# Optimization experiments

Hardware: AMD Instinct MI355X
Metric: run time of the kernel (lower is better)

## Reference

```python
import jax, jax.numpy as jnp
import numpy as np

B, N, S, D1, D2 = 8, 16384, 1024, 256, 256
C_IN, C_MID, C_OUT = D1 + D2, 256, 256
BN_EPS = 1e-5
DIST_EPS = 1e-8


def setup_inputs() -> dict:
    key = jax.random.key(0)
    ks = jax.random.split(key, 12)
    return {
        "xyz1": jax.random.normal(ks[0], (B, 3, N), jnp.float32),
        "xyz2": jax.random.normal(ks[1], (B, 3, S), jnp.float32),
        "points1": jax.random.normal(ks[2], (B, D1, N), jnp.float32),
        "points2": jax.random.normal(ks[3], (B, D2, S), jnp.float32),
        "w0": jax.random.normal(ks[4], (C_MID, C_IN), jnp.float32) * (1.0 / np.sqrt(C_IN)),
        "b0": jnp.zeros((C_MID,), jnp.float32),
        "g0": jnp.ones((C_MID,), jnp.float32),
        "be0": jnp.zeros((C_MID,), jnp.float32),
        "w1": jax.random.normal(ks[5], (C_OUT, C_MID), jnp.float32) * (1.0 / np.sqrt(C_MID)),
        "b1": jnp.zeros((C_OUT,), jnp.float32),
        "g1": jnp.ones((C_OUT,), jnp.float32),
        "be1": jnp.zeros((C_OUT,), jnp.float32),
    }


def _propagate(xyz1, xyz2, points1, points2):
    # xyz1 [B,3,N], xyz2 [B,3,S], points1 [B,D1,N], points2 [B,D2,S]
    x1 = jnp.transpose(xyz1, (0, 2, 1))   # [B,N,3]
    x2 = jnp.transpose(xyz2, (0, 2, 1))   # [B,S,3]
    p2 = jnp.transpose(points2, (0, 2, 1))  # [B,S,D2]
    # squared pairwise distances [B,N,S]
    d = (jnp.sum(x1 * x1, -1, keepdims=True)
         - 2.0 * jnp.einsum('bnc,bsc->bns', x1, x2)
         + jnp.sum(x2 * x2, -1)[:, None, :])
    neg_d, idx = jax.lax.top_k(-d, 3)     # 3 nearest neighbors
    dist = -neg_d                          # [B,N,3]
    recip = 1.0 / (dist + DIST_EPS)
    w = recip / jnp.sum(recip, -1, keepdims=True)  # [B,N,3]
    gathered = jax.vmap(lambda feats, ids: feats[ids])(p2, idx)  # [B,N,3,D2]
    interp = jnp.sum(gathered * w[..., None], axis=2)            # [B,N,D2]
    p1 = jnp.transpose(points1, (0, 2, 1))  # [B,N,D1]
    new = jnp.concatenate([p1, interp], axis=-1)  # [B,N,D1+D2]
    return jnp.transpose(new, (0, 2, 1))          # [B,C_IN,N]


def _conv_bn_relu(x, w, b, g, be):
    # 1x1 conv as matmul; BN in training mode (batch stats over B and N)
    y = jnp.einsum('oc,bcn->bon', w, x) + b[None, :, None]
    mean = jnp.mean(y, axis=(0, 2), keepdims=True)
    var = jnp.var(y, axis=(0, 2), keepdims=True)
    y = (y - mean) * jax.lax.rsqrt(var + BN_EPS)
    y = y * g[None, :, None] + be[None, :, None]
    return jax.nn.relu(y)


def reference(xyz1, xyz2, points1, points2, w0, b0, g0, be0, w1, b1, g1, be1):
    x = _propagate(xyz1, xyz2, points1, points2)  # [B,512,N]
    x = _conv_bn_relu(x, w0, b0, g0, be0)
    x = _conv_bn_relu(x, w1, b1, g1, be1)
    return x  # [B,256,N]
```

## Files before the change

kernel.cpp:

```cpp
#include <hip/hip_runtime.h>
#include <stdint.h>

#define BB    8
#define NN_   16384
#define SS    1024
#define PP    131072
#define CIN   512
#define CMID  256
#define COUT  256

typedef short  bf16x8 __attribute__((ext_vector_type(8)));
typedef float  f32x4  __attribute__((ext_vector_type(4)));
typedef unsigned short u16x8 __attribute__((ext_vector_type(8)));
typedef unsigned int uint_;

__device__ __forceinline__ float bf2f(unsigned short u){
  union { unsigned int i; float f; } v; v.i = ((unsigned int)u) << 16; return v.f;
}
__device__ __forceinline__ unsigned short f2bf(float f){
  union { float f; unsigned int i; } v; v.f = f;
  unsigned int r = (v.i + 0x7fffu + ((v.i >> 16) & 1u)) >> 16;
  return (unsigned short)r;
}

__device__ __forceinline__ void async_ld16(const void* g, void* l){
  const uint32_t __attribute__((address_space(1)))* gp =
    reinterpret_cast<const uint32_t __attribute__((address_space(1)))*>(reinterpret_cast<uintptr_t>(g));
  uint32_t __attribute__((address_space(3)))* lp =
    reinterpret_cast<uint32_t __attribute__((address_space(3)))*>(reinterpret_cast<uintptr_t>(l));
  __builtin_amdgcn_global_load_lds(gp, lp, 16, 0, 0);
}

__global__ void k_prep(const float* __restrict__ w0, const float* __restrict__ w1,
                       unsigned short* __restrict__ w0b, unsigned short* __restrict__ w1b,
                       float* __restrict__ bn)
{
  int idx = blockIdx.x * 256 + threadIdx.x;
  if (idx < 131072) w0b[idx] = f2bf(w0[idx]);
  if (idx < 65536)  w1b[idx] = f2bf(w1[idx]);
  if (idx < 2048)   bn[idx]  = 0.0f;
}

__global__ void k_p2t(const float* __restrict__ p2, float* __restrict__ p2t)
{
  __shared__ float t[32][33];
  const int b = blockIdx.z, c0 = blockIdx.y * 32, s0 = blockIdx.x * 32;
  const int tx = threadIdx.x, ty = threadIdx.y;
#pragma unroll
  for (int r = 0; r < 4; r++)
    t[ty + r*8][tx] = p2[((size_t)b*256 + c0 + ty + r*8) * SS + s0 + tx];
  __syncthreads();
#pragma unroll
  for (int r = 0; r < 4; r++)
    p2t[((size_t)b*SS + s0 + ty + r*8) * 256 + c0 + tx] = t[tx][ty + r*8];
}

__global__ void k_p1t(const float* __restrict__ p1, unsigned short* __restrict__ xcat)
{
  __shared__ float t[32][33];
  const int b = blockIdx.z, c0 = blockIdx.y * 32, n0 = blockIdx.x * 32;
  const int tx = threadIdx.x, ty = threadIdx.y;
#pragma unroll
  for (int r = 0; r < 4; r++)
    t[ty + r*8][tx] = p1[((size_t)b*256 + c0 + ty + r*8) * (size_t)NN_ + n0 + tx];
  __syncthreads();
#pragma unroll
  for (int r = 0; r < 4; r++)
    xcat[((size_t)b*NN_ + n0 + ty + r*8) * 512 + c0 + tx] = f2bf(t[tx][ty + r*8]);
}

__global__ __launch_bounds__(256) void k_nn(const float* __restrict__ xyz1,
                                            const float* __restrict__ xyz2,
                                            const float* __restrict__ p2t,
                                            unsigned short* __restrict__ xcat)
{
  __shared__ float4 pts[SS];
  __shared__ int4   mi[256];
  __shared__ float4 mw[256];
  const int blk = blockIdx.x;
  const int b = blk & 7, nt = blk >> 3;
  const int n0 = nt * 256, tid = threadIdx.x;

  for (int s = tid; s < SS; s += 256) {
    float x = xyz2[((size_t)b*3 + 0) * SS + s];
    float y = xyz2[((size_t)b*3 + 1) * SS + s];
    float z = xyz2[((size_t)b*3 + 2) * SS + s];
    pts[s] = make_float4(x, y, z, 0.0f);
  }
  __syncthreads();

  const int n = n0 + tid;
  const float qx = xyz1[((size_t)b*3 + 0) * NN_ + n];
  const float qy = xyz1[((size_t)b*3 + 1) * NN_ + n];
  const float qz = xyz1[((size_t)b*3 + 2) * NN_ + n];

  const float KINIT = __uint_as_float(0x7F7FFFFFu);
  float c0 = KINIT, c1 = KINIT, c2 = KINIT, c3 = KINIT, c4 = KINIT, c5 = KINIT;
#pragma unroll 4
  for (int s = 0; s < SS; s++) {
    float4 p = pts[s];
    float dx = qx - p.x, dy = qy - p.y, dz = qz - p.z;
    float d = fmaf(dx, dx, fmaf(dy, dy, dz * dz));
    float key = __uint_as_float((__float_as_uint(d) & 0xFFFFFC00u) | (uint_)s);
    float m0 = fminf(c0, key);
    float m1 = __builtin_amdgcn_fmed3f(c0, c1, key);
    float m2 = __builtin_amdgcn_fmed3f(c1, c2, key);
    float m3 = __builtin_amdgcn_fmed3f(c2, c3, key);
    float m4 = __builtin_amdgcn_fmed3f(c3, c4, key);
    float m5 = __builtin_amdgcn_fmed3f(c4, c5, key);
    c0 = m0; c1 = m1; c2 = m2; c3 = m3; c4 = m4; c5 = m5;
  }

  const double qxd = (double)qx, qyd = (double)qy, qzd = (double)qz;
  uint_  ks[6] = { __float_as_uint(c0), __float_as_uint(c1), __float_as_uint(c2),
                   __float_as_uint(c3), __float_as_uint(c4), __float_as_uint(c5) };
  int    ii[6];
  double dd[6];
#pragma unroll
  for (int t = 0; t < 6; t++) {
    ii[t] = (int)(ks[t] & 1023u);
    float4 p = pts[ii[t]];
    double dx = qxd - (double)p.x, dy = qyd - (double)p.y, dz = qzd - (double)p.z;
    dd[t] = dx*dx + dy*dy + dz*dz;
  }
#pragma unroll
  for (int a = 1; a < 6; a++)
#pragma unroll
    for (int c = a; c > 0; c--)
      if (dd[c] < dd[c-1]) {
        double td = dd[c]; dd[c] = dd[c-1]; dd[c-1] = td;
        int    ti = ii[c]; ii[c] = ii[c-1]; ii[c-1] = ti;
      }

  double r0 = 1.0/(dd[0] + 1e-8), r1 = 1.0/(dd[1] + 1e-8), r2 = 1.0/(dd[2] + 1e-8);
  double rs = 1.0/(r0 + r1 + r2);
  mi[tid] = make_int4(ii[0], ii[1], ii[2], 0);
  mw[tid] = make_float4((float)(r0*rs), (float)(r1*rs), (float)(r2*rs), 0.0f);
  __syncthreads();

  const int wid = tid >> 6, lane = tid & 63;
  const float* p2tb = p2t + (size_t)b * SS * 256;
  unsigned short* outb = xcat + ((size_t)b*NN_ + n0) * 512 + 256 + lane*4;
#pragma unroll 2
  for (int t = 0; t < 64; t++) {
    int j = wid*64 + t;
    int4   im = mi[j];
    float4 wm = mw[j];
    const float4* ra = (const float4*)(p2tb + (size_t)im.x * 256) + lane;
    const float4* rb = (const float4*)(p2tb + (size_t)im.y * 256) + lane;
    const float4* rc = (const float4*)(p2tb + (size_t)im.z * 256) + lane;
    float4 A = *ra, Bv = *rb, Cv = *rc;
    float fx = wm.x*A.x + wm.y*Bv.x + wm.z*Cv.x;
    float fy = wm.x*A.y + wm.y*Bv.y + wm.z*Cv.y;
    float fz = wm.x*A.z + wm.y*Bv.z + wm.z*Cv.z;
    float fw = wm.x*A.w + wm.y*Bv.w + wm.z*Cv.w;
    uint_ lo = (uint_)f2bf(fx) | ((uint_)f2bf(fy) << 16);
    uint_ hi = (uint_)f2bf(fz) | ((uint_)f2bf(fw) << 16);
    uint2 pk; pk.x = lo; pk.y = hi;
    *(uint2*)(outb + (size_t)j * 512) = pk;
  }
}

__global__ __launch_bounds__(512, 2) void k_gemm(const unsigned short* __restrict__ X,
                                                 const unsigned short* __restrict__ W,
                                                 unsigned short* __restrict__ Y,
                                                 float* __restrict__ bnsum,
                                                 float* __restrict__ bnsumsq,
                                                 int K)
{
  extern __shared__ char smem[];
  const int tid  = threadIdx.x;
  const int wid  = tid >> 6, lane = tid & 63;
  const int quad = lane >> 4, l16 = lane & 15;
  const int wp = wid >> 2, wo = wid & 3;
  const size_t p0 = (size_t)blockIdx.x * 256;

  f32x4 acc[8][4] = {};

  const int grow = (wid << 4) | (lane >> 2);
  const int gcol = (((lane & 3) ^ ((lane >> 3) & 3)) << 3);
  const unsigned short* gA0 = X + (p0 + grow)       * (size_t)K + gcol;
  const unsigned short* gA1 = X + (p0 + grow + 128) * (size_t)K + gcol;
  const unsigned short* gB0 = W + (size_t)(grow)       * K + gcol;
  const unsigned short* gB1 = W + (size_t)(grow + 128) * K + gcol;
  const int ldw = wid << 10;

  auto stage = [&](int t) {
    char* base = smem + ((t & 3) << 15);
    const int kk = t << 5;
    async_ld16(gA0 + kk, base + ldw);
    async_ld16(gA1 + kk, base + 8192 + ldw);
    async_ld16(gB0 + kk, base + 16384 + ldw);
    async_ld16(gB1 + kk, base + 16384 + 8192 + ldw);
  };

  const int sw   = (quad ^ ((l16 >> 1) & 3)) << 4;
  const int aoff = ((wp << 7) + l16) * 64 + sw;
  const int boff = ((wo << 6) + l16) * 64 + sw;

  const int nt = K >> 5;
  stage(0); stage(1); stage(2);
  asm volatile("s_waitcnt vmcnt(8)" ::: "memory");
  __builtin_amdgcn_s_barrier();

  for (int t = 0; t < nt; ++t) {
    const char* buf = smem + ((t & 3) << 15);
    bf16x8 af[8], bfr[4];
#pragma unroll
    for (int m = 0; m < 8; m++) af[m]  = *(const bf16x8*)(buf + aoff + m*1024);
#pragma unroll
    for (int n = 0; n < 4; n++) bfr[n] = *(const bf16x8*)(buf + 16384 + boff + n*1024);
    asm volatile("s_waitcnt lgkmcnt(0)" ::: "memory");
    __builtin_amdgcn_s_barrier();
    if (t + 3 < nt) stage(t + 3);
#pragma unroll
    for (int m = 0; m < 8; m++)
#pragma unroll
      for (int n = 0; n < 4; n++)
        acc[m][n] = __builtin_amdgcn_mfma_f32_16x16x32_bf16(af[m], bfr[n], acc[m][n], 0, 0, 0);
    if (t < nt - 1) {
      if (t + 3 < nt)      asm volatile("s_waitcnt vmcnt(8)" ::: "memory");
      else if (t + 2 < nt) asm volatile("s_waitcnt vmcnt(4)" ::: "memory");
      else                 asm volatile("s_waitcnt vmcnt(0)" ::: "memory");
      __builtin_amdgcn_s_barrier();
    }
  }

#pragma unroll
  for (int n = 0; n < 4; n++) {
    float s = 0.0f, ss = 0.0f;
#pragma unroll
    for (int m = 0; m < 8; m++)
#pragma unroll
      for (int i = 0; i < 4; i++) { float v = acc[m][n][i]; s += v; ss += v*v; }
    s  += __shfl_xor(s, 16, 64);  s  += __shfl_xor(s, 32, 64);
    ss += __shfl_xor(ss, 16, 64); ss += __shfl_xor(ss, 32, 64);
    if (quad == 0) {
      int o = (wo << 6) + (n << 4) + l16;
      atomicAdd(&bnsum[o], s);
      atomicAdd(&bnsumsq[o], ss);
    }
  }
#pragma unroll
  for (int m = 0; m < 8; m++)
#pragma unroll
    for (int n = 0; n < 4; n++)
#pragma unroll
      for (int i = 0; i < 4; i++) {
        size_t p = p0 + (wp << 7) + (m << 4) + (quad << 2) + i;
        int    o = (wo << 6) + (n << 4) + l16;
        Y[p * 256 + o] = f2bf(acc[m][n][i]);
      }
}

__global__ void k_bn(const float* __restrict__ sum, const float* __restrict__ sumsq,
                     const float* __restrict__ g, const float* __restrict__ be,
                     float* __restrict__ scale, float* __restrict__ shift)
{
  int o = threadIdx.x;
  const float inv = 1.0f / 131072.0f;
  float m  = sum[o] * inv;
  float v  = sumsq[o] * inv - m * m;
  float sc = g[o] * rsqrtf(v + 1e-5f);
  scale[o] = sc;
  shift[o] = be[o] - m * sc;
}

__global__ __launch_bounds__(256) void k_z(const unsigned short* __restrict__ y,
                                           const float* __restrict__ scale,
                                           const float* __restrict__ shift,
                                           unsigned short* __restrict__ z)
{
  size_t idx = ((size_t)blockIdx.x * 256 + threadIdx.x) * 8;
  int o = (int)(idx & 255);
  u16x8 v = *(const u16x8*)(y + idx);
  u16x8 r;
#pragma unroll
  for (int i = 0; i < 8; i++) {
    float f = bf2f(v[i]);
    float t = f * scale[o + i] + shift[o + i];
    r[i] = f2bf(fmaxf(t, 0.0f));
  }
  *(u16x8*)(z + idx) = r;
}

__global__ __launch_bounds__(256) void k_out(const unsigned short* __restrict__ y1,
                                             const float* __restrict__ scale,
                                             const float* __restrict__ shift,
                                             float* __restrict__ out)
{
  __shared__ float t[64][65];
  const int b = blockIdx.z, o0 = blockIdx.y * 64, n0 = blockIdx.x * 64;
  const int tx = threadIdx.x & 15, ty = threadIdx.x >> 4;
  const float4 sc = *(const float4*)(scale + o0 + tx*4);
  const float4 sh = *(const float4*)(shift + o0 + tx*4);
#pragma unroll
  for (int r = 0; r < 4; r++) {
    int nl = ty + r*16;
    const unsigned short* src = y1 + ((size_t)b*NN_ + n0 + nl) * 256 + o0 + tx*4;
    ushort4 v = *(const ushort4*)src;
    t[tx*4+0][nl] = fmaxf(bf2f(v.x) * sc.x + sh.x, 0.0f);
    t[tx*4+1][nl] = fmaxf(bf2f(v.y) * sc.y + sh.y, 0.0f);
    t[tx*4+2][nl] = fmaxf(bf2f(v.z) * sc.z + sh.z, 0.0f);
    t[tx*4+3][nl] = fmaxf(bf2f(v.w) * sc.w + sh.w, 0.0f);
  }
  __syncthreads();
#pragma unroll
  for (int r = 0; r < 4; r++) {
    int ol = ty + r*16;
    float4 o4 = make_float4(t[ol][tx*4+0], t[ol][tx*4+1], t[ol][tx*4+2], t[ol][tx*4+3]);
    *(float4*)(out + ((size_t)b*256 + o0 + ol) * (size_t)NN_ + n0 + tx*4) = o4;
  }
}

extern "C" void kernel_launch(void* const* d_in, const int* in_sizes, int n_in,
                              void* d_out, int out_size, void* d_ws, size_t ws_size,
                              hipStream_t stream)
{
  const float* xyz1 = (const float*)d_in[0];
  const float* xyz2 = (const float*)d_in[1];
  const float* p1   = (const float*)d_in[2];
  const float* p2   = (const float*)d_in[3];
  const float* w0   = (const float*)d_in[4];
  const float* g0   = (const float*)d_in[6];
  const float* be0  = (const float*)d_in[7];
  const float* w1   = (const float*)d_in[8];
  const float* g1   = (const float*)d_in[10];
  const float* be1  = (const float*)d_in[11];

  char* ws = (char*)d_ws;
  unsigned short* xcat = (unsigned short*)(ws);
  unsigned short* y0   = (unsigned short*)(ws + 134217728ull);
  unsigned short* zbuf = (unsigned short*)(ws);
  unsigned short* y1   = (unsigned short*)(ws + 67108864ull);
  float*          p2t  = (float*)        (ws + 134217728ull);
  unsigned short* w0b  = (unsigned short*)(ws + 201326592ull);
  unsigned short* w1b  = (unsigned short*)(ws + 201588736ull);
  float*          bn   = (float*)        (ws + 201719808ull);

  static bool s_init = false;
  if (!s_init) {
    hipFuncSetAttribute(reinterpret_cast<const void*>(&k_gemm),
                        hipFuncAttributeMaxDynamicSharedMemorySize, 131072);
    s_init = true;
  }

  k_prep<<<512, 256, 0, stream>>>(w0, w1, w0b, w1b, bn);
  k_p2t <<<dim3(32, 8, 8),  dim3(32, 8), 0, stream>>>(p2, p2t);
  k_p1t <<<dim3(512, 8, 8), dim3(32, 8), 0, stream>>>(p1, xcat);
  k_nn  <<<512, 256, 0, stream>>>(xyz1, xyz2, p2t, xcat);
  k_gemm<<<512, 512, 131072, stream>>>(xcat, w0b, y0, bn + 0,   bn + 256, 512);
  k_bn  <<<1, 256, 0, stream>>>(bn + 0,   bn + 256, g0, be0, bn + 1024, bn + 1280);
  k_z   <<<16384, 256, 0, stream>>>(y0, bn + 1024, bn + 1280, zbuf);
  k_gemm<<<512, 512, 131072, stream>>>(zbuf, w1b, y1, bn + 512, bn + 768, 256);
  k_bn  <<<1, 256, 0, stream>>>(bn + 512, bn + 768, g1, be1, bn + 1536, bn + 1792);
  k_out <<<dim3(256, 4, 8), 256, 0, stream>>>(y1, bn + 1536, bn + 1792, (float*)d_out);
}
```

Baseline: 510.7 us.

## Split NN search across two threads per query and widen GEMM blocks

The nearest-neighbour kernel now gives each query two threads. Each thread scans half of the 1024 reference points, and the two partial top-6 lists are merged through shared memory before the exact refinement. This doubles the block count so more waves can hide latency in the serial distance loop. The GEMM moves to 1024-thread blocks where each wave computes a 64x64 tile instead of 128x64, which lowers register pressure per wave. The cost is more LDS fragment loads per MFMA and tighter staging waits.

```diff
diff --git a/kernel.cpp b/kernel.cpp
--- a/kernel.cpp
+++ b/kernel.cpp
@@ -75,11 +75,13 @@
                                             unsigned short* __restrict__ xcat)
 {
   __shared__ float4 pts[SS];
-  __shared__ int4   mi[256];
-  __shared__ float4 mw[256];
+  __shared__ int4   mi[128];
+  __shared__ float4 mw[128];
+  __shared__ float  ck[128][6];
   const int blk = blockIdx.x;
   const int b = blk & 7, nt = blk >> 3;
-  const int n0 = nt * 256, tid = threadIdx.x;
+  const int n0 = nt * 128, tid = threadIdx.x;
+  const int tq = tid & 127, half = tid >> 7;
 
   for (int s = tid; s < SS; s += 256) {
     float x = xyz2[((size_t)b*3 + 0) * SS + s];
@@ -89,15 +91,16 @@
   }
   __syncthreads();
 
-  const int n = n0 + tid;
+  const int n = n0 + tq;
   const float qx = xyz1[((size_t)b*3 + 0) * NN_ + n];
   const float qy = xyz1[((size_t)b*3 + 1) * NN_ + n];
   const float qz = xyz1[((size_t)b*3 + 2) * NN_ + n];
 
   const float KINIT = __uint_as_float(0x7F7FFFFFu);
   float c0 = KINIT, c1 = KINIT, c2 = KINIT, c3 = KINIT, c4 = KINIT, c5 = KINIT;
+  const int s0 = half << 9;
 #pragma unroll 4
-  for (int s = 0; s < SS; s++) {
+  for (int s = s0; s < s0 + 512; s++) {
     float4 p = pts[s];
     float dx = qx - p.x, dy = qy - p.y, dz = qz - p.z;
     float d = fmaf(dx, dx, fmaf(dy, dy, dz * dz));
@@ -111,39 +114,59 @@
     c0 = m0; c1 = m1; c2 = m2; c3 = m3; c4 = m4; c5 = m5;
   }
 
-  const double qxd = (double)qx, qyd = (double)qy, qzd = (double)qz;
-  uint_  ks[6] = { __float_as_uint(c0), __float_as_uint(c1), __float_as_uint(c2),
-                   __float_as_uint(c3), __float_as_uint(c4), __float_as_uint(c5) };
-  int    ii[6];
-  double dd[6];
-#pragma unroll
-  for (int t = 0; t < 6; t++) {
-    ii[t] = (int)(ks[t] & 1023u);
-    float4 p = pts[ii[t]];
-    double dx = qxd - (double)p.x, dy = qyd - (double)p.y, dz = qzd - (double)p.z;
-    dd[t] = dx*dx + dy*dy + dz*dz;
-  }
-#pragma unroll
-  for (int a = 1; a < 6; a++)
-#pragma unroll
-    for (int c = a; c > 0; c--)
-      if (dd[c] < dd[c-1]) {
-        double td = dd[c]; dd[c] = dd[c-1]; dd[c-1] = td;
-        int    ti = ii[c]; ii[c] = ii[c-1]; ii[c-1] = ti;
-      }
-
-  double r0 = 1.0/(dd[0] + 1e-8), r1 = 1.0/(dd[1] + 1e-8), r2 = 1.0/(dd[2] + 1e-8);
-  double rs = 1.0/(r0 + r1 + r2);
-  mi[tid] = make_int4(ii[0], ii[1], ii[2], 0);
-  mw[tid] = make_float4((float)(r0*rs), (float)(r1*rs), (float)(r2*rs), 0.0f);
+  if (half) {
+    ck[tq][0] = c0; ck[tq][1] = c1; ck[tq][2] = c2;
+    ck[tq][3] = c3; ck[tq][4] = c4; ck[tq][5] = c5;
+  }
+  __syncthreads();
+
+  if (!half) {
+#pragma unroll
+    for (int j = 0; j < 6; j++) {
+      float key = ck[tq][j];
+      float m0 = fminf(c0, key);
+      float m1 = __builtin_amdgcn_fmed3f(c0, c1, key);
+      float m2 = __builtin_amdgcn_fmed3f(c1, c2, key);
+      float m3 = __builtin_amdgcn_fmed3f(c2, c3, key);
+      float m4 = __builtin_amdgcn_fmed3f(c3, c4, key);
+      float m5 = __builtin_amdgcn_fmed3f(c4, c5, key);
+      c0 = m0; c1 = m1; c2 = m2; c3 = m3; c4 = m4; c5 = m5;
+    }
+
+    const double qxd = (double)qx, qyd = (double)qy, qzd = (double)qz;
+    uint_  ks[6] = { __float_as_uint(c0), __float_as_uint(c1), __float_as_uint(c2),
+                     __float_as_uint(c3), __float_as_uint(c4), __float_as_uint(c5) };
+    int    ii[6];
+    double dd[6];
+#pragma unroll
+    for (int t = 0; t < 6; t++) {
+      ii[t] = (int)(ks[t] & 1023u);
+      float4 p = pts[ii[t]];
+      double dx = qxd - (double)p.x, dy = qyd - (double)p.y, dz = qzd - (double)p.z;
+      dd[t] = dx*dx + dy*dy + dz*dz;
+    }
+#pragma unroll
+    for (int a = 1; a < 6; a++)
+#pragma unroll
+      for (int c = a; c > 0; c--)
+        if (dd[c] < dd[c-1]) {
+          double td = dd[c]; dd[c] = dd[c-1]; dd[c-1] = td;
+          int    ti = ii[c]; ii[c] = ii[c-1]; ii[c-1] = ti;
+        }
+
+    double r0 = 1.0/(dd[0] + 1e-8), r1 = 1.0/(dd[1] + 1e-8), r2 = 1.0/(dd[2] + 1e-8);
+    double rs = 1.0/(r0 + r1 + r2);
+    mi[tq] = make_int4(ii[0], ii[1], ii[2], 0);
+    mw[tq] = make_float4((float)(r0*rs), (float)(r1*rs), (float)(r2*rs), 0.0f);
+  }
   __syncthreads();
 
   const int wid = tid >> 6, lane = tid & 63;
   const float* p2tb = p2t + (size_t)b * SS * 256;
   unsigned short* outb = xcat + ((size_t)b*NN_ + n0) * 512 + 256 + lane*4;
 #pragma unroll 2
-  for (int t = 0; t < 64; t++) {
-    int j = wid*64 + t;
+  for (int t = 0; t < 32; t++) {
+    int j = wid*32 + t;
     int4   im = mi[j];
     float4 wm = mw[j];
     const float4* ra = (const float4*)(p2tb + (size_t)im.x * 256) + lane;
@@ -161,12 +184,12 @@
   }
 }
 
-__global__ __launch_bounds__(512, 2) void k_gemm(const unsigned short* __restrict__ X,
-                                                 const unsigned short* __restrict__ W,
-                                                 unsigned short* __restrict__ Y,
-                                                 float* __restrict__ bnsum,
-                                                 float* __restrict__ bnsumsq,
-                                                 int K)
+__global__ __launch_bounds__(1024, 4) void k_gemm(const unsigned short* __restrict__ X,
+                                                  const unsigned short* __restrict__ W,
+                                                  unsigned short* __restrict__ Y,
+                                                  float* __restrict__ bnsum,
+                                                  float* __restrict__ bnsumsq,
+                                                  int K)
 {
   extern __shared__ char smem[];
   const int tid  = threadIdx.x;
@@ -175,52 +198,48 @@
   const int wp = wid >> 2, wo = wid & 3;
   const size_t p0 = (size_t)blockIdx.x * 256;
 
-  f32x4 acc[8][4] = {};
-
-  const int grow = (wid << 4) | (lane >> 2);
-  const int gcol = (((lane & 3) ^ ((lane >> 3) & 3)) << 3);
-  const unsigned short* gA0 = X + (p0 + grow)       * (size_t)K + gcol;
-  const unsigned short* gA1 = X + (p0 + grow + 128) * (size_t)K + gcol;
-  const unsigned short* gB0 = W + (size_t)(grow)       * K + gcol;
-  const unsigned short* gB1 = W + (size_t)(grow + 128) * K + gcol;
+  f32x4 acc[4][4] = {};
+
+  const int grow = tid >> 2;
+  const int gcol = (((tid & 3) ^ ((tid >> 3) & 3)) << 3);
+  const unsigned short* gA = X + (p0 + grow) * (size_t)K + gcol;
+  const unsigned short* gB = W + (size_t)grow * K + gcol;
   const int ldw = wid << 10;
 
   auto stage = [&](int t) {
     char* base = smem + ((t & 3) << 15);
     const int kk = t << 5;
-    async_ld16(gA0 + kk, base + ldw);
-    async_ld16(gA1 + kk, base + 8192 + ldw);
-    async_ld16(gB0 + kk, base + 16384 + ldw);
-    async_ld16(gB1 + kk, base + 16384 + 8192 + ldw);
+    async_ld16(gA + kk, base + ldw);
+    async_ld16(gB + kk, base + 16384 + ldw);
   };
 
   const int sw   = (quad ^ ((l16 >> 1) & 3)) << 4;
-  const int aoff = ((wp << 7) + l16) * 64 + sw;
+  const int aoff = ((wp << 6) + l16) * 64 + sw;
   const int boff = ((wo << 6) + l16) * 64 + sw;
 
   const int nt = K >> 5;
   stage(0); stage(1); stage(2);
-  asm volatile("s_waitcnt vmcnt(8)" ::: "memory");
+  asm volatile("s_waitcnt vmcnt(4)" ::: "memory");
   __builtin_amdgcn_s_barrier();
 
   for (int t = 0; t < nt; ++t) {
     const char* buf = smem + ((t & 3) << 15);
-    bf16x8 af[8], bfr[4];
-#pragma unroll
-    for (int m = 0; m < 8; m++) af[m]  = *(const bf16x8*)(buf + aoff + m*1024);
+    bf16x8 af[4], bfr[4];
+#pragma unroll
+    for (int m = 0; m < 4; m++) af[m]  = *(const bf16x8*)(buf + aoff + m*1024);
 #pragma unroll
     for (int n = 0; n < 4; n++) bfr[n] = *(const bf16x8*)(buf + 16384 + boff + n*1024);
     asm volatile("s_waitcnt lgkmcnt(0)" ::: "memory");
     __builtin_amdgcn_s_barrier();
     if (t + 3 < nt) stage(t + 3);
 #pragma unroll
-    for (int m = 0; m < 8; m++)
+    for (int m = 0; m < 4; m++)
 #pragma unroll
       for (int n = 0; n < 4; n++)
         acc[m][n] = __builtin_amdgcn_mfma_f32_16x16x32_bf16(af[m], bfr[n], acc[m][n], 0, 0, 0);
     if (t < nt - 1) {
-      if (t + 3 < nt)      asm volatile("s_waitcnt vmcnt(8)" ::: "memory");
-      else if (t + 2 < nt) asm volatile("s_waitcnt vmcnt(4)" ::: "memory");
+      if (t + 3 < nt)      asm volatile("s_waitcnt vmcnt(4)" ::: "memory");
+      else if (t + 2 < nt) asm volatile("s_waitcnt vmcnt(2)" ::: "memory");
       else                 asm volatile("s_waitcnt vmcnt(0)" ::: "memory");
       __builtin_amdgcn_s_barrier();
     }
@@ -230,7 +249,7 @@
   for (int n = 0; n < 4; n++) {
     float s = 0.0f, ss = 0.0f;
 #pragma unroll
-    for (int m = 0; m < 8; m++)
+    for (int m = 0; m < 4; m++)
 #pragma unroll
       for (int i = 0; i < 4; i++) { float v = acc[m][n][i]; s += v; ss += v*v; }
     s  += __shfl_xor(s, 16, 64);  s  += __shfl_xor(s, 32, 64);
@@ -242,12 +261,12 @@
     }
   }
 #pragma unroll
-  for (int m = 0; m < 8; m++)
+  for (int m = 0; m < 4; m++)
 #pragma unroll
     for (int n = 0; n < 4; n++)
 #pragma unroll
       for (int i = 0; i < 4; i++) {
-        size_t p = p0 + (wp << 7) + (m << 4) + (quad << 2) + i;
+        size_t p = p0 + (wp << 6) + (m << 4) + (quad << 2) + i;
         int    o = (wo << 6) + (n << 4) + l16;
         Y[p * 256 + o] = f2bf(acc[m][n][i]);
       }
@@ -348,11 +367,11 @@
   k_prep<<<512, 256, 0, stream>>>(w0, w1, w0b, w1b, bn);
   k_p2t <<<dim3(32, 8, 8),  dim3(32, 8), 0, stream>>>(p2, p2t);
   k_p1t <<<dim3(512, 8, 8), dim3(32, 8), 0, stream>>>(p1, xcat);
-  k_nn  <<<512, 256, 0, stream>>>(xyz1, xyz2, p2t, xcat);
-  k_gemm<<<512, 512, 131072, stream>>>(xcat, w0b, y0, bn + 0,   bn + 256, 512);
+  k_nn  <<<1024, 256, 0, stream>>>(xyz1, xyz2, p2t, xcat);
+  k_gemm<<<512, 1024, 131072, stream>>>(xcat, w0b, y0, bn + 0,   bn + 256, 512);
   k_bn  <<<1, 256, 0, stream>>>(bn + 0,   bn + 256, g0, be0, bn + 1024, bn + 1280);
   k_z   <<<16384, 256, 0, stream>>>(y0, bn + 1024, bn + 1280, zbuf);
-  k_gemm<<<512, 512, 131072, stream>>>(zbuf, w1b, y1, bn + 512, bn + 768, 256);
+  k_gemm<<<512, 1024, 131072, stream>>>(zbuf, w1b, y1, bn + 512, bn + 768, 256);
   k_bn  <<<1, 256, 0, stream>>>(bn + 512, bn + 768, g1, be1, bn + 1536, bn + 1792);
   k_out <<<dim3(256, 4, 8), 256, 0, stream>>>(y1, bn + 1536, bn + 1792, (float*)d_out);
 }
```

New measurement: 543.5 us. 1.06x slower.
